# Performance work log

Hardware: AMD Instinct MI355X
Metric: run time of the kernel (lower is better)

The kernel has to match this reference:

```python
import jax, jax.numpy as jnp
import numpy as np

B, N, D, N_HOPS = 32, 1024, 128, 3
EPS = 1e-6


def setup_inputs() -> dict:
    key = jax.random.key(0)
    k1, k2, k3, k4 = jax.random.split(key, 4)
    # binary base adjacency (non-trainable buffer in the torch module)
    adj = (jax.random.uniform(k1, (N, N)) < 0.05).astype(jnp.float32)
    adj_weight = jax.random.uniform(k2, (B, N, N), dtype=jnp.float32)
    x = jax.random.normal(k3, (B, N, D), dtype=jnp.float32)
    W = jax.random.normal(k4, (D, D), dtype=jnp.float32) * 0.05
    b = jnp.zeros((D,), jnp.float32)
    a2 = jnp.ones((D,), jnp.float32)   # LayerNorm scale
    b2 = jnp.zeros((D,), jnp.float32)  # LayerNorm shift
    return {"x": x, "adj_weight": adj_weight, "adj": adj, "W": W, "b": b, "a2": a2, "b2": b2}


def _conv(x, adj_weight, adj):
    # adj_power squares the matrix each hop: hop h uses A^(2^h).
    # mask_h = (A^(2^h) == 1.0); weighted hop = (W^(2^h)) * mask_h.
    # propagate(edge_index from dense_to_sparse) == sum_j Wmask[b,j,i] * x[b,j]  (A^T x)
    A = adj            # [N, N]
    Wp = adj_weight    # [B, N, N]
    agg = jnp.zeros_like(x)
    for h in range(N_HOPS):
        mask = (A == 1.0).astype(x.dtype)          # [N, N]
        Wh = Wp * mask                              # [B, N, N]
        agg = agg + jnp.einsum('bji,bjd->bid', Wh, x)
        if h < N_HOPS - 1:
            A = A @ A
            Wp = jnp.matmul(Wp, Wp)
    return agg


def reference(x, adj_weight, adj, W, b, a2, b2):
    agg = _conv(x, adj_weight, adj)
    h = jnp.einsum('bnd,od->bno', agg, W) + b + x   # Linear + residual
    mean = jnp.mean(h, axis=-1, keepdims=True)
    std = jnp.std(h, axis=-1, keepdims=True, ddof=1)  # torch.std is unbiased
    y = a2 * (h - mean) / (std + EPS) + b2
    return y  # dropout p=0 (eval) -> identity
```

## Files before the change

### kernel.cpp

```cpp
#include <hip/hip_runtime.h>

#define NN 1024
#define BB 32
#define DD 128
#define EPSF 1e-6f
#define CAP 16384
#define NNNN ((size_t)NN * NN)

typedef __bf16 bf16x8 __attribute__((ext_vector_type(8)));
typedef float  f32x4  __attribute__((ext_vector_type(4)));
typedef unsigned short u16x8 __attribute__((ext_vector_type(8)));

typedef __attribute__((address_space(3))) unsigned int lds_u32;
typedef __attribute__((address_space(1))) const unsigned int glb_u32;

__device__ __forceinline__ lds_u32* lds_cast(const void* p) {
  return (lds_u32*)(unsigned int)(unsigned long long)p;
}
__device__ __forceinline__ glb_u32* glb_cast(const void* p) {
  return (glb_u32*)(unsigned long long)p;
}

__device__ __forceinline__ float bf2f(unsigned short u) {
  union { unsigned int i; float f; } v; v.i = ((unsigned int)u) << 16; return v.f;
}
__device__ __forceinline__ unsigned short f2bf(float f) {
  union { float f; unsigned int i; } v; v.f = f;
  unsigned int r = v.i + 0x7fffu + ((v.i >> 16) & 1u);
  return (unsigned short)(r >> 16);
}


__global__ __launch_bounds__(256) void convert_wp(const float* __restrict__ src,
    unsigned short* __restrict__ Wp, unsigned short* __restrict__ WpT) {
  __shared__ float tile[64][65];
  const int b = blockIdx.z;
  const int c0 = blockIdx.x * 64, r0 = blockIdx.y * 64;
  const int t = threadIdx.x;
  const int rr = t >> 3, cb = (t & 7) * 8;
  const size_t base = (size_t)b * NNNN;
#pragma unroll
  for (int p = 0; p < 2; ++p) {
    const int r = rr + p * 32;
    const float* srow = src + base + (size_t)(r0 + r) * NN + c0 + cb;
    f32x4 v0 = *(const f32x4*)srow;
    f32x4 v1 = *(const f32x4*)(srow + 4);
    u16x8 w;
#pragma unroll
    for (int j = 0; j < 4; ++j) { w[j] = f2bf(v0[j]); w[4 + j] = f2bf(v1[j]); }
    *(u16x8*)(Wp + base + (size_t)(r0 + r) * NN + c0 + cb) = w;
#pragma unroll
    for (int j = 0; j < 4; ++j) { tile[r][cb + j] = v0[j]; tile[r][cb + 4 + j] = v1[j]; }
  }
  __syncthreads();
#pragma unroll
  for (int p = 0; p < 2; ++p) {
    const int r = rr + p * 32;
    u16x8 w;
#pragma unroll
    for (int j = 0; j < 8; ++j) w[j] = f2bf(tile[cb + j][r]);
    *(u16x8*)(WpT + base + (size_t)(c0 + r) * NN + r0 + cb) = w;
  }
}

__global__ __launch_bounds__(256) void convert_x(const float* __restrict__ x,
    unsigned short* __restrict__ xT) {
  __shared__ float tile[32][33];
  const int b = blockIdx.z;
  const int d0 = blockIdx.x * 32, n0 = blockIdx.y * 32;
  const int tx = threadIdx.x, ty = threadIdx.y;
#pragma unroll
  for (int s = 0; s < 4; ++s) {
    int rr = ty + s * 8;
    tile[rr][tx] = x[(size_t)b * NN * DD + (size_t)(n0 + rr) * DD + d0 + tx];
  }
  __syncthreads();
#pragma unroll
  for (int s = 0; s < 4; ++s) {
    int rr = ty + s * 8;
    xT[(size_t)b * DD * NN + (size_t)(d0 + rr) * NN + n0 + tx] = f2bf(tile[tx][rr]);
  }
}

__global__ __launch_bounds__(256) void mask0cvt(const float* __restrict__ adj,
    unsigned char* __restrict__ mcode, unsigned short* __restrict__ adjbf,
    unsigned short* __restrict__ adjTbf) {
  __shared__ float tile[32][33];
  const int i0 = blockIdx.x * 32, j0 = blockIdx.y * 32;
  const int tx = threadIdx.x, ty = threadIdx.y;
#pragma unroll
  for (int s = 0; s < 4; ++s) {
    int rr = ty + s * 8;
    float v = adj[(size_t)(j0 + rr) * NN + i0 + tx];
    adjbf[(size_t)(j0 + rr) * NN + i0 + tx] = f2bf(v);
    tile[rr][tx] = v;
  }
  __syncthreads();
#pragma unroll
  for (int s = 0; s < 4; ++s) {
    int rr = ty + s * 8;
    float v = tile[tx][rr];
    adjTbf[(size_t)(i0 + rr) * NN + j0 + tx] = f2bf(v);
    mcode[(size_t)(i0 + rr) * NN + j0 + tx] = (v == 1.0f) ? 1 : 0;
  }
}

__global__ __launch_bounds__(256) void scan_a2(const float* __restrict__ P,
    unsigned short* __restrict__ A2, unsigned short* __restrict__ A2T,
    unsigned char* __restrict__ mcode) {
  __shared__ float tile[32][33];
  const int m0 = blockIdx.x * 32, n0 = blockIdx.y * 32;
  const int tx = threadIdx.x, ty = threadIdx.y;
#pragma unroll
  for (int s = 0; s < 4; ++s) {
    int rr = ty + s * 8;
    size_t idx = (size_t)(m0 + rr) * NN + n0 + tx;
    float v = P[idx] + P[NNNN + idx] + P[2 * NNNN + idx] + P[3 * NNNN + idx];
    A2[idx] = f2bf(v);
    tile[rr][tx] = v;
  }
  __syncthreads();
#pragma unroll
  for (int s = 0; s < 4; ++s) {
    int rr = ty + s * 8;
    float v = tile[tx][rr];
    A2T[(size_t)(n0 + rr) * NN + m0 + tx] = f2bf(v);
    if (v == 1.0f) mcode[(size_t)(n0 + rr) * NN + m0 + tx] |= 2;
  }
}

__global__ __launch_bounds__(256) void scan_a4(const float* __restrict__ P,
    unsigned int* __restrict__ entries, int* __restrict__ nnz) {
  size_t e = (size_t)blockIdx.x * 256 + threadIdx.x;
  float v = P[e] + P[NNNN + e] + P[2 * NNNN + e] + P[3 * NNNN + e];
  if (v == 1.0f) {
    int idx = atomicAdd(nnz, 1);
    if (idx < CAP) entries[idx] = ((unsigned)(e >> 10) << 16) | (unsigned)(e & 1023);
  }
}

#define BM 128
#define BN 128
#define BK 32

struct EpiWcomb {
  const unsigned char* mc;
  unsigned short* out;
  __device__ __forceinline__ void operator()(int b, int ks, int i, int j, float v) const {
    size_t idx = (size_t)i * NN + j;
    out[(size_t)b * NNNN + idx] = (mc[idx] & 2) ? f2bf(v) : (unsigned short)0;
  }
};

struct EpiSqPart {
  float* buf;
  __device__ __forceinline__ void operator()(int b, int ks, int i, int j, float v) const {
    buf[(size_t)ks * NNNN + (size_t)i * NN + j] = v;
  }
};

struct EpiAggPart {
  float* p0;
  float* p1;
  __device__ __forceinline__ void operator()(int b, int ks, int i, int d, float v) const {
    (ks ? p1 : p0)[(size_t)b * NN * DD + (size_t)i * DD + d] = v;
  }
};

#define LGKM_BARRIER() do { \
  asm volatile("s_waitcnt lgkmcnt(0)" ::: "memory"); \
  __builtin_amdgcn_s_barrier(); \
  asm volatile("" ::: "memory"); } while (0)

template <int MW, typename Epi>
__global__ __launch_bounds__(256, MW) void gemm_lds(
    const unsigned short* __restrict__ Ap, size_t sA,
    const unsigned short* __restrict__ Bp, size_t sB,
    int swz, int ksN, int nit, Epi epi) {
  __shared__ __align__(16) unsigned short As[BM * BK];
  __shared__ __align__(16) unsigned short Bs[BN * BK];
  const int z = blockIdx.z;
  const int b = z / ksN, ks = z - b * ksN;
  const int kbase = ks * nit * BK;
  int bx = blockIdx.x, by = blockIdx.y;
  if (swz) {
    int lin = bx + (by << 3);
    int r = lin & 7, s = lin >> 3;
    bx = ((r & 3) << 1) | (s & 1);
    by = ((r >> 2) << 2) | (s >> 1);
  }
  const int tm = bx * BM, tn = by * BN;
  const unsigned short* Ab = Ap + (size_t)b * sA;
  const unsigned short* Bb = Bp + (size_t)b * sB;
  const int tid = threadIdx.x;
  const int w = tid >> 6, l = tid & 63;
  const int fr = l & 15, quad = l >> 4;
  const int moff = (w & 1) * 64, noff = (w >> 1) * 64;

  const int sr = l >> 2, ss = l & 3;
  const int r0 = w * 16 + sr;
  const int r1 = 64 + w * 16 + sr;
  const int kc0 = ss ^ ((r0 >> 1) & 3);
  const int kc1 = ss ^ ((r1 >> 1) & 3);
  const unsigned short* gA0 = Ab + (size_t)(tm + r0) * NN + kbase + kc0 * 8;
  const unsigned short* gA1 = Ab + (size_t)(tm + r1) * NN + kbase + kc1 * 8;
  const unsigned short* gB0 = Bb + (size_t)(tn + r0) * NN + kbase + kc0 * 8;
  const unsigned short* gB1 = Bb + (size_t)(tn + r1) * NN + kbase + kc1 * 8;
  lds_u32* const lA0 = lds_cast(As + (w * 16) * BK);
  lds_u32* const lA1 = lds_cast(As + (64 + w * 16) * BK);
  lds_u32* const lB0 = lds_cast(Bs + (w * 16) * BK);
  lds_u32* const lB1 = lds_cast(Bs + (64 + w * 16) * BK);

  f32x4 acc[4][4];
#pragma unroll
  for (int mi = 0; mi < 4; ++mi)
#pragma unroll
    for (int ni = 0; ni < 4; ++ni) acc[mi][ni] = (f32x4){0.f, 0.f, 0.f, 0.f};

#pragma unroll 1
  for (int kt = 0; kt < nit; ++kt) {
    const size_t kk = (size_t)kt * BK;
    __builtin_amdgcn_global_load_lds(glb_cast(gA0 + kk), lA0, 16, 0, 0);
    __builtin_amdgcn_global_load_lds(glb_cast(gA1 + kk), lA1, 16, 0, 0);
    __builtin_amdgcn_global_load_lds(glb_cast(gB0 + kk), lB0, 16, 0, 0);
    __builtin_amdgcn_global_load_lds(glb_cast(gB1 + kk), lB1, 16, 0, 0);
    __syncthreads();
    bf16x8 af[4], bfr[4];
#pragma unroll
    for (int mi = 0; mi < 4; ++mi) {
      int r = moff + mi * 16 + fr;
      int kc = quad ^ ((r >> 1) & 3);
      af[mi] = *(const bf16x8*)(As + r * BK + kc * 8);
    }
#pragma unroll
    for (int ni = 0; ni < 4; ++ni) {
      int r = noff + ni * 16 + fr;
      int kc = quad ^ ((r >> 1) & 3);
      bfr[ni] = *(const bf16x8*)(Bs + r * BK + kc * 8);
    }
#pragma unroll
    for (int mi = 0; mi < 4; ++mi)
#pragma unroll
      for (int ni = 0; ni < 4; ++ni)
        acc[mi][ni] = __builtin_amdgcn_mfma_f32_16x16x32_bf16(af[mi], bfr[ni], acc[mi][ni], 0, 0, 0);
    __syncthreads();
  }

#pragma unroll
  for (int mi = 0; mi < 4; ++mi)
#pragma unroll
    for (int ni = 0; ni < 4; ++ni)
#pragma unroll
      for (int t = 0; t < 4; ++t)
        epi(b, ks, tm + moff + mi * 16 + quad * 4 + t, tn + noff + ni * 16 + fr, acc[mi][ni][t]);
}

template <int MW, bool COMB, typename Epi>
__global__ __launch_bounds__(256, MW) void gemm_pipe(
    const unsigned short* __restrict__ Ap, size_t sA,
    const unsigned short* __restrict__ WtP, const unsigned char* __restrict__ McP,
    const unsigned short* __restrict__ Bp, size_t sB,
    int swz, int ksN, int nit, Epi epi) {
  __shared__ __align__(16) unsigned short As[2 * BM * BK];
  __shared__ __align__(16) unsigned short Bs[2 * BN * BK];
  const int z = blockIdx.z;
  const int b = z / ksN, ks = z - b * ksN;
  const int kbase = ks * nit * BK;
  int bx = blockIdx.x, by = blockIdx.y;
  if (swz) {
    int lin = bx + (by << 3);
    int r = lin & 7, s = lin >> 3;
    bx = ((r & 3) << 1) | (s & 1);
    by = ((r >> 2) << 2) | (s >> 1);
  }
  const int tm = bx * BM, tn = by * BN;
  const unsigned short* Ab = Ap + (size_t)b * sA;
  const unsigned short* Bb = Bp + (size_t)b * sB;
  const unsigned short* Wb = COMB ? (WtP + (size_t)b * sA) : nullptr;
  const int tid = threadIdx.x;
  const int w = tid >> 6, l = tid & 63;
  const int lr = l >> 2, lc = l & 3;
  const int fr = l & 15, quad = l >> 4;
  const int moff = (w & 1) * 64, noff = (w >> 1) * 64;
  const int r0 = w * 16 + lr, r1 = (w + 4) * 16 + lr;
  const int kc0 = lc ^ ((r0 >> 1) & 3), kc1 = lc ^ ((r1 >> 1) & 3);
  const size_t ao0 = (size_t)(tm + r0) * NN + kbase + kc0 * 8;
  const size_t ao1 = (size_t)(tm + r1) * NN + kbase + kc1 * 8;
  const size_t bo0 = (size_t)(tn + r0) * NN + kbase + kc0 * 8;
  const size_t bo1 = (size_t)(tn + r1) * NN + kbase + kc1 * 8;
  const int ls0 = r0 * BK + lc * 8, ls1 = r1 * BK + lc * 8;

  unsigned short* const As0 = As;           unsigned short* const As1 = As + BM * BK;
  unsigned short* const Bs0 = Bs;           unsigned short* const Bs1 = Bs + BN * BK;

  f32x4 acc[4][4];
#pragma unroll
  for (int mi = 0; mi < 4; ++mi)
#pragma unroll
    for (int ni = 0; ni < 4; ++ni) acc[mi][ni] = (f32x4){0.f, 0.f, 0.f, 0.f};

  struct RegSet {
    u16x8 a0, a1, b0, b1;
    u16x8 w0, w1;
    unsigned long long m0, m1;
  };
  RegSet R0, R1;

  auto load = [&](RegSet& R, int kt) {
    size_t kk = (size_t)kt * BK;
    R.a0 = *(const u16x8*)(Ab + ao0 + kk);
    R.a1 = *(const u16x8*)(Ab + ao1 + kk);
    R.b0 = *(const u16x8*)(Bb + bo0 + kk);
    R.b1 = *(const u16x8*)(Bb + bo1 + kk);
    if constexpr (COMB) {
      R.w0 = *(const u16x8*)(Wb + ao0 + kk);
      R.w1 = *(const u16x8*)(Wb + ao1 + kk);
      R.m0 = *(const unsigned long long*)(McP + ao0 + kk);
      R.m1 = *(const unsigned long long*)(McP + ao1 + kk);
    }
  };
  auto wr = [&](const RegSet& R, unsigned short* Ad, unsigned short* Bd) {
    if constexpr (COMB) {
      u16x8 f0, f1;
#pragma unroll
      for (int j = 0; j < 8; ++j) {
        float s0 = bf2f(R.a0[j]);
        if ((R.m0 >> (8 * j)) & 1ull) s0 += bf2f(R.w0[j]);
        f0[j] = f2bf(s0);
        float s1 = bf2f(R.a1[j]);
        if ((R.m1 >> (8 * j)) & 1ull) s1 += bf2f(R.w1[j]);
        f1[j] = f2bf(s1);
      }
      *(u16x8*)(Ad + ls0) = f0;
      *(u16x8*)(Ad + ls1) = f1;
    } else {
      *(u16x8*)(Ad + ls0) = R.a0;
      *(u16x8*)(Ad + ls1) = R.a1;
    }
    *(u16x8*)(Bd + ls0) = R.b0;
    *(u16x8*)(Bd + ls1) = R.b1;
  };
  auto compute = [&](const unsigned short* Ad, const unsigned short* Bd) {
    bf16x8 af[4], bfr[4];
#pragma unroll
    for (int mi = 0; mi < 4; ++mi) {
      int r = moff + mi * 16 + fr;
      int kc = quad ^ ((r >> 1) & 3);
      af[mi] = *(const bf16x8*)(Ad + r * BK + kc * 8);
    }
#pragma unroll
    for (int ni = 0; ni < 4; ++ni) {
      int r = noff + ni * 16 + fr;
      int kc = quad ^ ((r >> 1) & 3);
      bfr[ni] = *(const bf16x8*)(Bd + r * BK + kc * 8);
    }
#pragma unroll
    for (int mi = 0; mi < 4; ++mi)
#pragma unroll
      for (int ni = 0; ni < 4; ++ni)
        acc[mi][ni] = __builtin_amdgcn_mfma_f32_16x16x32_bf16(af[mi], bfr[ni], acc[mi][ni], 0, 0, 0);
  };

  load(R0, 0);
  load(R1, 1);
  wr(R0, As0, Bs0);
  load(R0, 2);
  LGKM_BARRIER();
#pragma unroll 1
  for (int kt = 0; kt < nit - 2; kt += 2) {
    compute(As0, Bs0);
    wr(R1, As1, Bs1);
    if (kt + 3 < nit) load(R1, kt + 3);
    LGKM_BARRIER();
    compute(As1, Bs1);
    wr(R0, As0, Bs0);
    if (kt + 4 < nit) load(R0, kt + 4);
    LGKM_BARRIER();
  }
  compute(As0, Bs0);
  wr(R1, As1, Bs1);
  LGKM_BARRIER();
  compute(As1, Bs1);

#pragma unroll
  for (int mi = 0; mi < 4; ++mi)
#pragma unroll
    for (int ni = 0; ni < 4; ++ni)
#pragma unroll
      for (int t = 0; t < 4; ++t)
        epi(b, ks, tm + moff + mi * 16 + quad * 4 + t, tn + noff + ni * 16 + fr, acc[mi][ni][t]);
}

__global__ __launch_bounds__(256) void hop2_fix(const unsigned short* __restrict__ Wp,
    const unsigned short* __restrict__ WpT, const int* __restrict__ nnz,
    const unsigned int* __restrict__ entries, unsigned short* __restrict__ WcombT) {
  int n = *nnz;
  if (n > CAP) n = CAP;
  if (n == 0) return;
  __shared__ float rbuf[256];
  const int b = blockIdx.x;
  const size_t bnn = (size_t)b * NNNN;
  for (int e = blockIdx.y; e < n; e += gridDim.y) {
    unsigned int ent = entries[e];
    int j = ent >> 16, i = ent & 0xFFFF;
    float s = 0.f;
    for (int k = threadIdx.x; k < NN; k += 256) {
      float u = 0.f, v = 0.f;
      const unsigned short* wj  = Wp  + bnn + (size_t)j * NN;
      const unsigned short* wtk = WpT + bnn + (size_t)k * NN;
      const unsigned short* wk  = Wp  + bnn + (size_t)k * NN;
      const unsigned short* wti = WpT + bnn + (size_t)i * NN;
      for (int t = 0; t < NN; ++t) {
        u += bf2f(wj[t]) * bf2f(wtk[t]);
        v += bf2f(wk[t]) * bf2f(wti[t]);
      }
      s += u * v;
    }
    rbuf[threadIdx.x] = s;
    __syncthreads();
    for (int off = 128; off > 0; off >>= 1) {
      if (threadIdx.x < off) rbuf[threadIdx.x] += rbuf[threadIdx.x + off];
      __syncthreads();
    }
    if (threadIdx.x == 0) {
      size_t idx = bnn + (size_t)i * NN + j;
      WcombT[idx] = f2bf(bf2f(WcombT[idx]) + rbuf[0]);
    }
    __syncthreads();
  }
}

#define FROWS 16
__global__ __launch_bounds__(256) void fused_out(const float* __restrict__ a0p,
    const float* __restrict__ a1p, const float* __restrict__ x,
    const float* __restrict__ W, const float* __restrict__ bias,
    const float* __restrict__ g2, const float* __restrict__ bsh,
    float* __restrict__ out) {
  __shared__ unsigned short Wl[128 * 136];
  __shared__ float ar[256];
  __shared__ float wred[8];
  const int tid = threadIdx.x;
  for (int e = tid; e < 16384; e += 256) Wl[(e >> 7) * 136 + (e & 127)] = f2bf(W[e]);
  const int half = tid >> 7, o = tid & 127;
  const int w = tid >> 6, lane = tid & 63;
  const float bo = bias[o], go = g2[o], b2o = bsh[o];
  const size_t row0 = (size_t)blockIdx.x * FROWS;
  size_t rb = row0 * DD;
  float av = a0p[rb + tid] + a1p[rb + tid];
  float xv = x[rb + tid];
  __syncthreads();
  for (int rr = 0; rr < FROWS; rr += 2) {
    ar[tid] = av;
    const float xcur = xv;
    const size_t rbc = (row0 + rr) * DD;
    __syncthreads();
    if (rr + 2 < FROWS) {
      size_t rb2 = (row0 + rr + 2) * DD;
      av = a0p[rb2 + tid] + a1p[rb2 + tid];
      xv = x[rb2 + tid];
    }
    float hv = bo + xcur;
    const unsigned short* wrow = &Wl[o * 136];
    const float* arow = &ar[half * 128];
#pragma unroll
    for (int d8 = 0; d8 < 16; ++d8) {
      bf16x8 wv = *(const bf16x8*)(wrow + d8 * 8);
#pragma unroll
      for (int t = 0; t < 8; ++t) hv += (float)wv[t] * arow[d8 * 8 + t];
    }
    float s = hv, q = hv * hv;
#pragma unroll
    for (int off = 32; off > 0; off >>= 1) {
      s += __shfl_xor(s, off);
      q += __shfl_xor(q, off);
    }
    if (lane == 0) { wred[w] = s; wred[4 + w] = q; }
    __syncthreads();
    float st = wred[half * 2] + wred[half * 2 + 1];
    float qt = wred[4 + half * 2] + wred[4 + half * 2 + 1];
    float mean = st * (1.0f / 128.0f);
    float var = (qt - 128.0f * mean * mean) * (1.0f / 127.0f);
    var = fmaxf(var, 0.0f);
    float stdv = sqrtf(var);
    out[rbc + tid] = go * (hv - mean) / (stdv + EPSF) + b2o;
  }
}

extern "C" void kernel_launch(void* const* d_in, const int* in_sizes, int n_in,
                              void* d_out, int out_size, void* d_ws, size_t ws_size,
                              hipStream_t stream) {
  (void)in_sizes; (void)n_in; (void)out_size; (void)ws_size;
  const float* x    = (const float*)d_in[0];
  const float* adjw = (const float*)d_in[1];
  const float* adj  = (const float*)d_in[2];
  const float* W    = (const float*)d_in[3];
  const float* bias = (const float*)d_in[4];
  const float* a2   = (const float*)d_in[5];
  const float* b2   = (const float*)d_in[6];
  float* out = (float*)d_out;

  char* ws = (char*)d_ws;
  const size_t MB = 1048576;
  unsigned short* Wp_bf   = (unsigned short*)(ws);
  unsigned short* WpT_bf  = (unsigned short*)(ws + 64 * MB);
  unsigned short* WcombT  = (unsigned short*)(ws + 128 * MB);
  unsigned short* xT_bf   = (unsigned short*)(ws + 192 * MB);
  unsigned short* adj_bf  = (unsigned short*)(ws + 200 * MB);
  unsigned short* adjT_bf = (unsigned short*)(ws + 202 * MB);
  unsigned short* A2_bf   = (unsigned short*)(ws + 204 * MB);
  unsigned short* A2T_bf  = (unsigned short*)(ws + 206 * MB);
  float* sqpart           = (float*)(ws + 208 * MB);
  float* agg1             = (float*)(ws + 200 * MB);
  unsigned char* mcode    = (unsigned char*)(ws + 224 * MB);
  unsigned int* entries   = (unsigned int*)(ws + 225 * MB);
  int* nnz2               = (int*)(ws + 226 * MB);
  float* agg0 = out;

  hipMemsetAsync(nnz2, 0, 4, stream);

  dim3 blk32(32, 8, 1);
  convert_wp<<<dim3(16, 16, 32), 256, 0, stream>>>(adjw, Wp_bf, WpT_bf);
  convert_x<<<dim3(4, 32, 32), blk32, 0, stream>>>(x, xT_bf);
  mask0cvt<<<dim3(32, 32, 1), blk32, 0, stream>>>(adj, mcode, adj_bf, adjT_bf);

  gemm_lds<4><<<dim3(8, 8, 4), 256, 0, stream>>>(
      adj_bf, (size_t)0, adjT_bf, (size_t)0, 0, 4, 8, EpiSqPart{sqpart});
  scan_a2<<<dim3(32, 32, 1), blk32, 0, stream>>>(sqpart, A2_bf, A2T_bf, mcode);
  gemm_lds<4><<<dim3(8, 8, 4), 256, 0, stream>>>(
      A2_bf, (size_t)0, A2T_bf, (size_t)0, 0, 4, 8, EpiSqPart{sqpart});
  scan_a4<<<dim3(4096, 1, 1), 256, 0, stream>>>(sqpart, entries, nnz2);

  gemm_lds<4><<<dim3(8, 8, 32), 256, 0, stream>>>(
      WpT_bf, NNNN, Wp_bf, NNNN, 1, 1, NN / BK, EpiWcomb{mcode, WcombT});

  hop2_fix<<<dim3(32, 8, 1), 256, 0, stream>>>(Wp_bf, WpT_bf, nnz2, entries, WcombT);

  gemm_pipe<2, true><<<dim3(8, 1, 64), 256, 0, stream>>>(
      WcombT, NNNN, WpT_bf, mcode, xT_bf, (size_t)DD * NN, 0, 2, 16,
      EpiAggPart{agg0, agg1});

  fused_out<<<dim3(2048, 1, 1), 256, 0, stream>>>(agg0, agg1, x, W, bias, a2, b2, out);
}
```

Measured before the change: 478.7 us.

## Double-buffer LDS in gemm_lds and add XCD-aware block remapping

The single-buffered gemm_lds loop becomes double-buffered: the next K tile is loaded into a second LDS buffer while the current one is computed, which hides global-load latency behind MFMA work. A new swizzle mode (swz==2) remaps block ids so that blocks dispatched round-robin to the same XCD share a batch, which should improve L2 locality for the batched Wp^2 GEMM and the aggregation GEMM. LDS use in gemm_lds doubles, which may reduce occupancy at the 4-wave launch bound.

```diff
diff --git a/kernel.cpp b/kernel.cpp
--- a/kernel.cpp
+++ b/kernel.cpp
@@ -177,18 +177,23 @@
     const unsigned short* __restrict__ Ap, size_t sA,
     const unsigned short* __restrict__ Bp, size_t sB,
     int swz, int ksN, int nit, Epi epi) {
-  __shared__ __align__(16) unsigned short As[BM * BK];
-  __shared__ __align__(16) unsigned short Bs[BN * BK];
-  const int z = blockIdx.z;
-  const int b = z / ksN, ks = z - b * ksN;
-  const int kbase = ks * nit * BK;
-  int bx = blockIdx.x, by = blockIdx.y;
-  if (swz) {
+  __shared__ __align__(16) unsigned short As[2 * BM * BK];
+  __shared__ __align__(16) unsigned short Bs[2 * BN * BK];
+  int bx = blockIdx.x, by = blockIdx.y, z = blockIdx.z;
+  if (swz == 1) {
     int lin = bx + (by << 3);
     int r = lin & 7, s = lin >> 3;
     bx = ((r & 3) << 1) | (s & 1);
     by = ((r >> 2) << 2) | (s >> 1);
-  }
+  } else if (swz == 2) {
+    int lin = bx + (by << 3) + (z << 6);
+    int xcd = lin & 7, q = lin >> 3;
+    z = xcd + ((q >> 6) << 3);
+    int tile = q & 63;
+    bx = tile & 7; by = tile >> 3;
+  }
+  const int b = z / ksN, ks = z - b * ksN;
+  const int kbase = ks * nit * BK;
   const int tm = bx * BM, tn = by * BN;
   const unsigned short* Ab = Ap + (size_t)b * sA;
   const unsigned short* Bb = Bp + (size_t)b * sB;
@@ -206,10 +211,16 @@
   const unsigned short* gA1 = Ab + (size_t)(tm + r1) * NN + kbase + kc1 * 8;
   const unsigned short* gB0 = Bb + (size_t)(tn + r0) * NN + kbase + kc0 * 8;
   const unsigned short* gB1 = Bb + (size_t)(tn + r1) * NN + kbase + kc1 * 8;
-  lds_u32* const lA0 = lds_cast(As + (w * 16) * BK);
-  lds_u32* const lA1 = lds_cast(As + (64 + w * 16) * BK);
-  lds_u32* const lB0 = lds_cast(Bs + (w * 16) * BK);
-  lds_u32* const lB1 = lds_cast(Bs + (64 + w * 16) * BK);
+  lds_u32* const lA0_0 = lds_cast(As + (w * 16) * BK);
+  lds_u32* const lA1_0 = lds_cast(As + (64 + w * 16) * BK);
+  lds_u32* const lB0_0 = lds_cast(Bs + (w * 16) * BK);
+  lds_u32* const lB1_0 = lds_cast(Bs + (64 + w * 16) * BK);
+  lds_u32* const lA0_1 = lds_cast(As + BM * BK + (w * 16) * BK);
+  lds_u32* const lA1_1 = lds_cast(As + BM * BK + (64 + w * 16) * BK);
+  lds_u32* const lB0_1 = lds_cast(Bs + BN * BK + (w * 16) * BK);
+  lds_u32* const lB1_1 = lds_cast(Bs + BN * BK + (64 + w * 16) * BK);
+  const unsigned short* const As0 = As;            const unsigned short* const As1 = As + BM * BK;
+  const unsigned short* const Bs0 = Bs;            const unsigned short* const Bs1 = Bs + BN * BK;
 
   f32x4 acc[4][4];
 #pragma unroll
@@ -217,33 +228,48 @@
 #pragma unroll
     for (int ni = 0; ni < 4; ++ni) acc[mi][ni] = (f32x4){0.f, 0.f, 0.f, 0.f};
 
-#pragma unroll 1
-  for (int kt = 0; kt < nit; ++kt) {
+  auto stage = [&](lds_u32* a0, lds_u32* a1, lds_u32* b0, lds_u32* b1, int kt) {
     const size_t kk = (size_t)kt * BK;
-    __builtin_amdgcn_global_load_lds(glb_cast(gA0 + kk), lA0, 16, 0, 0);
-    __builtin_amdgcn_global_load_lds(glb_cast(gA1 + kk), lA1, 16, 0, 0);
-    __builtin_amdgcn_global_load_lds(glb_cast(gB0 + kk), lB0, 16, 0, 0);
-    __builtin_amdgcn_global_load_lds(glb_cast(gB1 + kk), lB1, 16, 0, 0);
-    __syncthreads();
+    __builtin_amdgcn_global_load_lds(glb_cast(gA0 + kk), a0, 16, 0, 0);
+    __builtin_amdgcn_global_load_lds(glb_cast(gA1 + kk), a1, 16, 0, 0);
+    __builtin_amdgcn_global_load_lds(glb_cast(gB0 + kk), b0, 16, 0, 0);
+    __builtin_amdgcn_global_load_lds(glb_cast(gB1 + kk), b1, 16, 0, 0);
+  };
+  auto compute = [&](const unsigned short* Ad, const unsigned short* Bd) {
     bf16x8 af[4], bfr[4];
 #pragma unroll
     for (int mi = 0; mi < 4; ++mi) {
       int r = moff + mi * 16 + fr;
       int kc = quad ^ ((r >> 1) & 3);
-      af[mi] = *(const bf16x8*)(As + r * BK + kc * 8);
+      af[mi] = *(const bf16x8*)(Ad + r * BK + kc * 8);
     }
 #pragma unroll
     for (int ni = 0; ni < 4; ++ni) {
       int r = noff + ni * 16 + fr;
       int kc = quad ^ ((r >> 1) & 3);
-      bfr[ni] = *(const bf16x8*)(Bs + r * BK + kc * 8);
+      bfr[ni] = *(const bf16x8*)(Bd + r * BK + kc * 8);
     }
 #pragma unroll
     for (int mi = 0; mi < 4; ++mi)
 #pragma unroll
       for (int ni = 0; ni < 4; ++ni)
         acc[mi][ni] = __builtin_amdgcn_mfma_f32_16x16x32_bf16(af[mi], bfr[ni], acc[mi][ni], 0, 0, 0);
+  };
+
+  stage(lA0_0, lA1_0, lB0_0, lB1_0, 0);
+  __syncthreads();
+#pragma unroll 1
+  for (int kt = 0; kt < nit; kt += 2) {
+    if (kt + 1 < nit) stage(lA0_1, lA1_1, lB0_1, lB1_1, kt + 1);
+    __builtin_amdgcn_sched_barrier(0);
+    compute(As0, Bs0);
     __syncthreads();
+    if (kt + 1 < nit) {
+      if (kt + 2 < nit) stage(lA0_0, lA1_0, lB0_0, lB1_0, kt + 2);
+      __builtin_amdgcn_sched_barrier(0);
+      compute(As1, Bs1);
+      __syncthreads();
+    }
   }
 
 #pragma unroll
@@ -263,16 +289,20 @@
     int swz, int ksN, int nit, Epi epi) {
   __shared__ __align__(16) unsigned short As[2 * BM * BK];
   __shared__ __align__(16) unsigned short Bs[2 * BN * BK];
-  const int z = blockIdx.z;
-  const int b = z / ksN, ks = z - b * ksN;
-  const int kbase = ks * nit * BK;
-  int bx = blockIdx.x, by = blockIdx.y;
-  if (swz) {
+  int bx = blockIdx.x, by = blockIdx.y, z = blockIdx.z;
+  if (swz == 1) {
     int lin = bx + (by << 3);
     int r = lin & 7, s = lin >> 3;
     bx = ((r & 3) << 1) | (s & 1);
     by = ((r >> 2) << 2) | (s >> 1);
-  }
+  } else if (swz == 2) {
+    int lin = bx + (z << 3);
+    int xcd = lin & 7, q = lin >> 3;
+    z = (xcd << 3) + (q >> 3);
+    bx = q & 7;
+  }
+  const int b = z / ksN, ks = z - b * ksN;
+  const int kbase = ks * nit * BK;
   const int tm = bx * BM, tn = by * BN;
   const unsigned short* Ab = Ap + (size_t)b * sA;
   const unsigned short* Bb = Bp + (size_t)b * sB;
@@ -531,12 +561,12 @@
   scan_a4<<<dim3(4096, 1, 1), 256, 0, stream>>>(sqpart, entries, nnz2);
 
   gemm_lds<4><<<dim3(8, 8, 32), 256, 0, stream>>>(
-      WpT_bf, NNNN, Wp_bf, NNNN, 1, 1, NN / BK, EpiWcomb{mcode, WcombT});
+      WpT_bf, NNNN, Wp_bf, NNNN, 2, 1, NN / BK, EpiWcomb{mcode, WcombT});
 
   hop2_fix<<<dim3(32, 8, 1), 256, 0, stream>>>(Wp_bf, WpT_bf, nnz2, entries, WcombT);
 
   gemm_pipe<2, true><<<dim3(8, 1, 64), 256, 0, stream>>>(
-      WcombT, NNNN, WpT_bf, mcode, xT_bf, (size_t)DD * NN, 0, 2, 16,
+      WcombT, NNNN, WpT_bf, mcode, xT_bf, (size_t)DD * NN, 2, 2, 16,
       EpiAggPart{agg0, agg1});
 
   fused_out<<<dim3(2048, 1, 1), 256, 0, stream>>>(agg0, agg1, x, W, bias, a2, b2, out);
```

Measured after the change: 464.3 us. 3.0% less time.
